# Kernel tuning notes

Measured on AMD Instinct MI355X. Metric: run time of the kernel, lower is better.

Reference implementation:

```python
import jax, jax.numpy as jnp
import numpy as np
import math

B, S, D, L, FF = 16, 2048, 512, 4, 2048
VOCAB, ATTR_VOCAB, MAXPOS = 33, 608, 2048
EPS = 1e-5


def layernorm(x, w, b):
    mu = jnp.mean(x, axis=-1, keepdims=True)
    var = jnp.mean(jnp.square(x - mu), axis=-1, keepdims=True)
    return (x - mu) * jax.lax.rsqrt(var + EPS) * w + b


def setup_inputs() -> dict:
    key = jax.random.key(0)
    ks = jax.random.split(key, 16)
    std = 0.02
    return {
        "input_ids": jax.random.randint(ks[0], (B, S), 0, VOCAB),
        "combined_indices": jax.random.randint(ks[1], (B,), 0, ATTR_VOCAB),
        "attention_mask": jnp.ones((B, S), dtype=jnp.float32),
        "tok_emb": jax.random.normal(ks[2], (VOCAB, D), jnp.float32) * std,
        "pos_emb": jax.random.normal(ks[3], (MAXPOS, D), jnp.float32) * std,
        "attr_emb": jax.random.normal(ks[4], (ATTR_VOCAB, D), jnp.float32) * std,
        "ln_w": jnp.ones((L, D), jnp.float32),
        "ln_b": jnp.zeros((L, D), jnp.float32),
        "w1": jax.random.normal(ks[5], (L, D, FF), jnp.float32) * std,
        "b1": jnp.zeros((L, FF), jnp.float32),
        "w2": jax.random.normal(ks[6], (L, FF, D), jnp.float32) * std,
        "b2": jnp.zeros((L, D), jnp.float32),
        "out_w": jax.random.normal(ks[7], (D, VOCAB), jnp.float32) * std,
        "out_b": jnp.zeros((VOCAB,), jnp.float32),
    }


def reference(input_ids, combined_indices, attention_mask, tok_emb, pos_emb,
              attr_emb, ln_w, ln_b, w1, b1, w2, b2, out_w, out_b):
    scale = 1.0 / math.sqrt(D)
    # embeddings: token + position + per-example attribute (broadcast over seq)
    x = tok_emb[input_ids] + pos_emb[jnp.arange(S)][None, :, :] \
        + attr_emb[combined_indices][:, None, :]
    mask_add = (1.0 - attention_mask)[:, None, :] * -1e9  # [B,1,S]
    for l in range(L):
        h = layernorm(x, ln_w[l], ln_b[l])                 # shared LN params used twice
        scores = jnp.einsum('bsd,btd->bst', h, h) * scale + mask_add
        probs = jax.nn.softmax(scores, axis=-1)            # dropout=0 (eval)
        attn = jnp.einsum('bst,btd->bsd', probs, h) + x    # residual
        n2 = layernorm(attn, ln_w[l], ln_b[l])
        ff = jax.nn.gelu(n2 @ w1[l] + b1[l], approximate=False) @ w2[l] + b2[l]
        x = ff + attn
    return x @ out_w + out_b
```

## Files before the change

kernel.cpp:

```cpp
#include <hip/hip_runtime.h>
#include <hip/hip_bf16.h>
#include <cmath>

#define B_ 16
#define S_ 2048
#define D_ 512
#define L_ 4
#define FF_ 2048
#define V_ 33

typedef unsigned short u16;
typedef __attribute__((ext_vector_type(8))) short bf16x8;
typedef __attribute__((ext_vector_type(4))) float f32x4;

__device__ __forceinline__ u16 f2bf(float f) {
    unsigned x = __float_as_uint(f);
    unsigned r = (x + 0x7fffu + ((x >> 16) & 1u)) >> 16;
    return (u16)r;
}
__device__ __forceinline__ float bf2f(u16 u) { return __uint_as_float(((unsigned)u) << 16); }

__device__ __forceinline__ float wave_sum(float v) {
#pragma unroll
    for (int o = 32; o; o >>= 1) v += __shfl_xor(v, o);
    return v;
}

__device__ __forceinline__ void gload16(const u16* g, u16* l) {
    __builtin_amdgcn_global_load_lds((const __attribute__((address_space(1))) void*)g,
                                     (__attribute__((address_space(3))) void*)l, 16, 0, 0);
}

__device__ __forceinline__ uint4 pack8(const u16* ov) {
    uint4 p;
    p.x = (unsigned)ov[0] | ((unsigned)ov[1] << 16);
    p.y = (unsigned)ov[2] | ((unsigned)ov[3] << 16);
    p.z = (unsigned)ov[4] | ((unsigned)ov[5] << 16);
    p.w = (unsigned)ov[6] | ((unsigned)ov[7] << 16);
    return p;
}

__global__ __launch_bounds__(256) void embed_kernel(
    const int* __restrict__ ids, const int* __restrict__ attr,
    const float* __restrict__ tok, const float* __restrict__ pos,
    const float* __restrict__ attre, float* __restrict__ x)
{
    int idx = blockIdx.x * 256 + threadIdx.x;
    const int total = B_ * S_ * (D_ / 4);
    if (idx >= total) return;
    int d4 = idx & (D_ / 4 - 1);
    int bs = idx >> 7;
    int s  = bs & (S_ - 1);
    int b  = bs >> 11;
    int id = ids[bs];
    int a  = attr[b];
    float4 t  = ((const float4*)tok)[id * (D_ / 4) + d4];
    float4 p  = ((const float4*)pos)[s * (D_ / 4) + d4];
    float4 at = ((const float4*)attre)[a * (D_ / 4) + d4];
    float4 o;
    o.x = t.x + p.x + at.x; o.y = t.y + p.y + at.y;
    o.z = t.z + p.z + at.z; o.w = t.w + p.w + at.w;
    ((float4*)x)[idx] = o;
}

__global__ __launch_bounds__(256) void ln_kernel(
    const float* __restrict__ in, u16* __restrict__ out,
    const float* __restrict__ w, const float* __restrict__ b, int rows)
{
    int gw = (int)((blockIdx.x * 256 + threadIdx.x) >> 6);
    int lane = threadIdx.x & 63;
    if (gw >= rows) return;
    const float4* p = (const float4*)(in + (size_t)gw * D_);
    float4 a0 = p[lane * 2], a1 = p[lane * 2 + 1];
    float xv[8] = {a0.x, a0.y, a0.z, a0.w, a1.x, a1.y, a1.z, a1.w};
    float s = 0.f;
#pragma unroll
    for (int k = 0; k < 8; k++) s += xv[k];
    s = wave_sum(s);
    float mu = s * (1.f / D_);
    float q = 0.f;
#pragma unroll
    for (int k = 0; k < 8; k++) { float d = xv[k] - mu; q += d * d; }
    q = wave_sum(q);
    float rs = rsqrtf(q * (1.f / D_) + 1e-5f);
    const float4* w4 = (const float4*)w;
    const float4* b4 = (const float4*)b;
    float4 w0 = w4[lane * 2], w1v = w4[lane * 2 + 1];
    float4 b0 = b4[lane * 2], b1v = b4[lane * 2 + 1];
    float wv[8] = {w0.x, w0.y, w0.z, w0.w, w1v.x, w1v.y, w1v.z, w1v.w};
    float bv[8] = {b0.x, b0.y, b0.z, b0.w, b1v.x, b1v.y, b1v.z, b1v.w};
    u16 ov[8];
#pragma unroll
    for (int k = 0; k < 8; k++) ov[k] = f2bf((xv[k] - mu) * rs * wv[k] + bv[k]);
    *(uint4*)(out + (size_t)gw * D_ + lane * 8) = pack8(ov);
}

#define LTS 66
__global__ __launch_bounds__(1024) void lnT_kernel(
    const float* __restrict__ in, u16* __restrict__ h, u16* __restrict__ hT,
    const float* __restrict__ w, const float* __restrict__ b)
{
    __shared__ u16 tile[512 * LTS];
    const int tid = threadIdx.x, lane = tid & 63, wv = tid >> 6;
    const int rb = blockIdx.x;
    const int z  = rb >> 5;
    const int s0 = (rb & 31) * 64;

    float wv8[8], bv8[8];
#pragma unroll
    for (int k = 0; k < 8; k++) {
        wv8[k] = w[k * 64 + lane];
        bv8[k] = b[k * 64 + lane];
    }

#pragma unroll
    for (int i = 0; i < 4; i++) {
        const int rl = wv * 4 + i;
        const size_t grow = (size_t)rb * 64 + rl;
        const float* xr = in + grow * D_;
        float xv[8];
#pragma unroll
        for (int k = 0; k < 8; k++) xv[k] = xr[k * 64 + lane];
        float s = 0.f;
#pragma unroll
        for (int k = 0; k < 8; k++) s += xv[k];
        s = wave_sum(s);
        float mu = s * (1.f / D_);
        float q = 0.f;
#pragma unroll
        for (int k = 0; k < 8; k++) { float d = xv[k] - mu; q += d * d; }
        q = wave_sum(q);
        float rs = rsqrtf(q * (1.f / D_) + 1e-5f);
        u16* hr = h + grow * D_;
#pragma unroll
        for (int k = 0; k < 8; k++) {
            u16 v = f2bf((xv[k] - mu) * rs * wv8[k] + bv8[k]);
            hr[k * 64 + lane] = v;
            tile[(k * 64 + lane) * LTS + rl] = v;
        }
    }
    __syncthreads();
    u16* hb = hT + (size_t)z * S_ * D_;
#pragma unroll
    for (int it = 0; it < 4; it++) {
        int idx = it * 1024 + tid;
        int d = idx >> 3, sg = (idx & 7) << 3;
        u16 v[8];
#pragma unroll
        for (int i = 0; i < 8; i++) v[i] = tile[d * LTS + sg + i];
        *(uint4*)(hb + (size_t)d * S_ + s0 + sg) = pack8(v);
    }
}

__device__ __forceinline__ void ld2(const float* p, int idx, u16& a, u16& b) {
    float2 v = ((const float2*)p)[idx];
    a = f2bf(v.x); b = f2bf(v.y);
}
__device__ __forceinline__ void ld2(const u16* p, int idx, u16& a, u16& b) {
    unsigned v = ((const unsigned*)p)[idx];
    a = (u16)(v & 0xffff); b = (u16)(v >> 16);
}

template <typename T>
__global__ void transpose64(const T* __restrict__ in, u16* __restrict__ out,
                            int R, int C, size_t sIn, size_t sOut)
{
    __shared__ u16 tile[64][66];
    const T* ip = in + (size_t)blockIdx.z * sIn;
    u16* op = out + (size_t)blockIdx.z * sOut;
    const int tx = threadIdx.x, ty = threadIdx.y;
#pragma unroll
    for (int i = 0; i < 8; i++) {
        int r = blockIdx.y * 64 + ty + i * 8;
        u16 a, b;
        ld2(ip + (size_t)r * C, blockIdx.x * 32 + tx, a, b);
        tile[tx * 2 + 0][ty + i * 8] = a;
        tile[tx * 2 + 1][ty + i * 8] = b;
    }
    __syncthreads();
#pragma unroll
    for (int i = 0; i < 8; i++) {
        int ocl = ty + i * 8;
        int oc  = blockIdx.x * 64 + ocl;
        unsigned w = (unsigned)tile[ocl][tx * 2] | ((unsigned)tile[ocl][tx * 2 + 1] << 16);
        ((unsigned*)(op + (size_t)oc * R + blockIdx.y * 64))[tx] = w;
    }
}

enum { E_PV = 1, E_GELU = 2, E_FF2 = 3 };

template <int EPI>
__global__ __launch_bounds__(256) void gemm_nt(
    const u16* __restrict__ A, size_t sAz, int lda,
    const u16* __restrict__ B, size_t sBz, int ldb,
    float* Cf, u16* Cb, size_t sCz, int ldc,
    int K, float scale,
    const float* resid, size_t sRz,
    const float* __restrict__ bias,
    const float* __restrict__ aux, int b0)
{
    __shared__ __align__(16) u16 ldsA[128 * 64];
    __shared__ __align__(16) u16 ldsB[128 * 64];
    __shared__ float l2[EPI == E_PV ? 128 : 1][2];

    const int gx = gridDim.x, gy = gridDim.y;
    const int nwg = gx * gy * gridDim.z;
    int lid = blockIdx.x + gx * (blockIdx.y + gy * blockIdx.z);
    {
        const int q = nwg >> 3, r = nwg & 7;
        const int xcd = lid & 7, idx = lid >> 3;
        lid = (xcd < r ? xcd * (q + 1) : r * (q + 1) + (xcd - r) * q) + idx;
    }
    const int bx = lid % gx;
    const int t2 = lid / gx;
    const int by = t2 % gy;
    const int z  = t2 / gy;

    A += (size_t)z * sAz;
    B += (size_t)z * sBz;
    const size_t coff = (size_t)z * sCz;
    const int brow = by * 128, bcol = bx * 128;
    const int tid = threadIdx.x, lane = tid & 63, wid = tid >> 6;
    const int wr = wid >> 1, wc = wid & 1;

    if constexpr (EPI == E_PV) {
        const int nrows = b0;
        const int base = z * S_ + brow;
        const int r = tid >> 1, ih = (tid & 1) << 4;
        float s = 0.f;
#pragma unroll
        for (int i = 0; i < 16; i++)
            s += aux[(size_t)(ih + i) * nrows + base + r];
        l2[r][tid & 1] = s;
    }

    f32x4 acc[4][4];
#pragma unroll
    for (int m = 0; m < 4; m++)
#pragma unroll
        for (int n = 0; n < 4; n++) acc[m][n] = 0.0f;

    const int lg   = lane >> 3;
    const int srow = wid * 8 + lg;
    const int skk  = ((lane & 7) ^ lg) << 3;
    const int l15 = lane & 15, l7 = lane & 7, kh = lane >> 4;

    for (int k0 = 0; k0 < K; k0 += 64) {
        __syncthreads();
#pragma unroll
        for (int r = 0; r < 4; r++) {
            const u16* ga = A + (size_t)(brow + r * 32 + srow) * lda + (k0 + skk);
            const u16* gb = B + (size_t)(bcol + r * 32 + srow) * ldb + (k0 + skk);
            gload16(ga, &ldsA[r * 2048 + wid * 512]);
            gload16(gb, &ldsB[r * 2048 + wid * 512]);
        }
        __syncthreads();
#pragma unroll
        for (int kk = 0; kk < 64; kk += 32) {
            const int kc = (kk >> 3) + kh;
            const int kswz = ((kc ^ l7) << 3);
            bf16x8 af[4], bfv[4];
#pragma unroll
            for (int m = 0; m < 4; m++)
                af[m] = *(const bf16x8*)&ldsA[(wr * 64 + m * 16 + l15) * 64 + kswz];
#pragma unroll
            for (int n = 0; n < 4; n++)
                bfv[n] = *(const bf16x8*)&ldsB[(wc * 64 + n * 16 + l15) * 64 + kswz];
#pragma unroll
            for (int m = 0; m < 4; m++)
#pragma unroll
                for (int n = 0; n < 4; n++)
                    acc[m][n] = __builtin_amdgcn_mfma_f32_16x16x32_bf16(af[m], bfv[n], acc[m][n], 0, 0, 0);
        }
    }

#pragma unroll
    for (int m = 0; m < 4; m++)
#pragma unroll
        for (int n = 0; n < 4; n++) {
            int rowb = brow + wr * 64 + m * 16 + ((lane >> 4) << 2);
            int col  = bcol + wc * 64 + n * 16 + l15;
#pragma unroll
            for (int j = 0; j < 4; j++) {
                int row = rowb + j;
                float v = acc[m][n][j];
                size_t off = coff + (size_t)row * ldc + col;
                if constexpr (EPI == E_PV) {
                    int rl = row - brow;
                    float lv = l2[rl][0] + l2[rl][1];
                    Cf[off] = v / lv + resid[(size_t)z * sRz + (size_t)row * ldc + col];
                } else if constexpr (EPI == E_GELU) {
                    float t = v + bias[col];
                    Cb[off] = f2bf(0.5f * t * (1.f + erff(t * 0.70710678118f)));
                } else {
                    Cf[off] = v + bias[col] + resid[(size_t)row * ldc + col];
                }
            }
        }
}

__global__ __launch_bounds__(256) void gemm_sc(
    const u16* __restrict__ h, u16* __restrict__ P,
    const float* __restrict__ mask, int b0, float scale,
    float* __restrict__ psum, int nbatch)
{
    __shared__ __align__(16) u16 ldsbuf[2][128 * 64];
    u16* ldsA = ldsbuf[0];
    u16* ldsB = ldsbuf[1];
    u16* mt   = &ldsbuf[0][0];

    const int nwg = 136 * nbatch;
    int lid = blockIdx.x + 136 * blockIdx.z;
    {
        const int q = nwg >> 3, r = nwg & 7;
        const int xcd = lid & 7, idx = lid >> 3;
        lid = (xcd < r ? xcd * (q + 1) : r * (q + 1) + (xcd - r) * q) + idx;
    }
    int t = lid % 136;
    const int z = lid / 136;
    int by = 0;
#pragma unroll 1
    while (t >= 16 - by) { t -= 16 - by; by++; }
    const int bx = by + t;

    const u16* A = h + (size_t)z * S_ * D_;
    const size_t coff = (size_t)z * S_ * S_;
    const int brow = by * 128, bcol = bx * 128;
    const int tid = threadIdx.x, lane = tid & 63, wid = tid >> 6;
    const int wr = wid >> 1, wc = wid & 1;

    f32x4 acc[4][4];
#pragma unroll
    for (int m = 0; m < 4; m++)
#pragma unroll
        for (int n = 0; n < 4; n++) acc[m][n] = 0.0f;

    const int lg   = lane >> 3;
    const int srow = wid * 8 + lg;
    const int skk  = ((lane & 7) ^ lg) << 3;
    const int l15 = lane & 15, l7 = lane & 7, kh = lane >> 4;

    for (int k0 = 0; k0 < D_; k0 += 64) {
        __syncthreads();
#pragma unroll
        for (int r = 0; r < 4; r++) {
            const u16* ga = A + (size_t)(brow + r * 32 + srow) * D_ + (k0 + skk);
            const u16* gb = A + (size_t)(bcol + r * 32 + srow) * D_ + (k0 + skk);
            gload16(ga, &ldsA[r * 2048 + wid * 512]);
            gload16(gb, &ldsB[r * 2048 + wid * 512]);
        }
        __syncthreads();
#pragma unroll
        for (int kk = 0; kk < 64; kk += 32) {
            const int kc = (kk >> 3) + kh;
            const int kswz = ((kc ^ l7) << 3);
            bf16x8 af[4], bfv[4];
#pragma unroll
            for (int m = 0; m < 4; m++)
                af[m] = *(const bf16x8*)&ldsA[(wr * 64 + m * 16 + l15) * 64 + kswz];
#pragma unroll
            for (int n = 0; n < 4; n++)
                bfv[n] = *(const bf16x8*)&ldsB[(wc * 64 + n * 16 + l15) * 64 + kswz];
#pragma unroll
            for (int m = 0; m < 4; m++)
#pragma unroll
                for (int n = 0; n < 4; n++)
                    acc[m][n] = __builtin_amdgcn_mfma_f32_16x16x32_bf16(af[m], bfv[n], acc[m][n], 0, 0, 0);
        }
    }

    const float* mrow = mask + (size_t)(b0 + z) * S_;
    const int nrows = nbatch * S_;

    float rsum[4][4];
#pragma unroll
    for (int m = 0; m < 4; m++)
#pragma unroll
        for (int j = 0; j < 4; j++) rsum[m][j] = 0.f;

#pragma unroll
    for (int m = 0; m < 4; m++)
#pragma unroll
        for (int n = 0; n < 4; n++) {
            int rowb = brow + wr * 64 + m * 16 + (kh << 2);
            int col  = bcol + wc * 64 + n * 16 + l15;
            float madd_c = (1.f - mrow[col]) * -1e9f;
#pragma unroll
            for (int j = 0; j < 4; j++) {
                int row = rowb + j;
                float ev = __expf(acc[m][n][j] * scale + madd_c);
                P[coff + (size_t)row * S_ + col] = f2bf(ev);
                rsum[m][j] += ev;
            }
        }
#pragma unroll
    for (int m = 0; m < 4; m++) {
        int rowl = brow + wr * 64 + m * 16 + (kh << 2);
#pragma unroll
        for (int j = 0; j < 4; j++) {
            float s = rsum[m][j];
            s += __shfl_xor(s, 1);
            s += __shfl_xor(s, 2);
            s += __shfl_xor(s, 4);
            s += __shfl_xor(s, 8);
            if (l15 == 0)
                psum[(size_t)(bx * 2 + wc) * nrows + (size_t)z * S_ + rowl + j] = s;
        }
    }

    if (bx != by) {
#pragma unroll 1
        for (int rnd = 0; rnd < 2; rnd++) {
            __syncthreads();
            if (wc == rnd) {
#pragma unroll
                for (int n = 0; n < 4; n++) {
                    float csum = 0.f;
                    const int mrow_l = n * 16 + l15;
#pragma unroll
                    for (int m = 0; m < 4; m++) {
                        const int lr = wr * 64 + m * 16 + (kh << 2);
                        u16 e2[4];
#pragma unroll
                        for (int j = 0; j < 4; j++) {
                            float madd_r = (1.f - mrow[brow + lr + j]) * -1e9f;
                            float em = __expf(acc[m][n][j] * scale + madd_r);
                            csum += em;
                            e2[j] = f2bf(em);
                        }
                        unsigned* m32 = (unsigned*)&mt[mrow_l * 136 + lr];
                        m32[0] = (unsigned)e2[0] | ((unsigned)e2[1] << 16);
                        m32[1] = (unsigned)e2[2] | ((unsigned)e2[3] << 16);
                    }
                    csum += __shfl_xor(csum, 16);
                    csum += __shfl_xor(csum, 32);
                    if (lane < 16)
                        psum[(size_t)(by * 2 + wr) * nrows + (size_t)z * S_ +
                             bcol + rnd * 64 + n * 16 + lane] = csum;
                }
            }
            __syncthreads();
#pragma unroll 1
            for (int i = tid; i < 64 * 16; i += 256) {
                int rr = i >> 4, c16 = (i & 15) << 3;
                u16 v[8];
#pragma unroll
                for (int q = 0; q < 8; q++) v[q] = mt[rr * 136 + c16 + q];
                *(uint4*)(P + coff + (size_t)(bcol + rnd * 64 + rr) * S_ + brow + c16) = pack8(v);
            }
        }
    }
}

__global__ __launch_bounds__(256) void wtb_kernel(
    const float* __restrict__ W, u16* __restrict__ WTb)
{
    int i = blockIdx.x * 256 + threadIdx.x;
    if (i >= 64 * 512) return;
    int n = i >> 9, k = i & 511;
    WTb[i] = f2bf(n < V_ ? W[k * V_ + n] : 0.f);
}

__global__ __launch_bounds__(256) void outproj_mfma(
    const float* __restrict__ x, const u16* __restrict__ WTb,
    const float* __restrict__ bias, float* __restrict__ out)
{
    __shared__ __align__(16) u16 ldsA[128 * 64];
    __shared__ __align__(16) u16 ldsB[64 * 64];
    __shared__ float obuf[128][34];
    const int brow = blockIdx.x * 128;
    const int tid = threadIdx.x, lane = tid & 63, wid = tid >> 6;
    const int wr = wid >> 1, wc = wid & 1;
    const int l15 = lane & 15, l7 = lane & 7, kh = lane >> 4;
    const int lg = lane >> 3, srow = wid * 8 + lg;
    const int skk = ((lane & 7) ^ lg) << 3;
    const int ar = tid >> 1, ah = (tid & 1) * 32;

    f32x4 acc[4][2];
#pragma unroll
    for (int m = 0; m < 4; m++)
#pragma unroll
        for (int n = 0; n < 2; n++) acc[m][n] = 0.0f;

    for (int k0 = 0; k0 < 512; k0 += 64) {
        __syncthreads();
#pragma unroll
        for (int r = 0; r < 2; r++)
            gload16(WTb + (size_t)(r * 32 + srow) * 512 + (k0 + skk),
                    &ldsB[r * 2048 + wid * 512]);
        const float4* xs = (const float4*)(x + (size_t)(brow + ar) * 512 + k0 + ah);
#pragma unroll
        for (int j = 0; j < 4; j++) {
            float4 a = xs[j * 2], b = xs[j * 2 + 1];
            u16 t[8] = {f2bf(a.x), f2bf(a.y), f2bf(a.z), f2bf(a.w),
                        f2bf(b.x), f2bf(b.y), f2bf(b.z), f2bf(b.w)};
            int kc = (ah >> 3) + j;
            *(uint4*)&ldsA[ar * 64 + ((kc ^ (ar & 7)) << 3)] = pack8(t);
        }
        __syncthreads();
#pragma unroll
        for (int kk = 0; kk < 64; kk += 32) {
            const int kc = (kk >> 3) + kh;
            const int kswz = ((kc ^ l7) << 3);
            bf16x8 af[4], bfv[2];
#pragma unroll
            for (int m = 0; m < 4; m++)
                af[m] = *(const bf16x8*)&ldsA[(wr * 64 + m * 16 + l15) * 64 + kswz];
#pragma unroll
            for (int n = 0; n < 2; n++)
                bfv[n] = *(const bf16x8*)&ldsB[(wc * 32 + n * 16 + l15) * 64 + kswz];
#pragma unroll
            for (int m = 0; m < 4; m++)
#pragma unroll
                for (int n = 0; n < 2; n++)
                    acc[m][n] = __builtin_amdgcn_mfma_f32_16x16x32_bf16(af[m], bfv[n], acc[m][n], 0, 0, 0);
        }
    }

#pragma unroll
    for (int m = 0; m < 4; m++)
#pragma unroll
        for (int n = 0; n < 2; n++) {
            int rowl = wr * 64 + m * 16 + ((lane >> 4) << 2);
            int col  = wc * 32 + n * 16 + l15;
            if (col < V_) {
#pragma unroll
                for (int j = 0; j < 4; j++)
                    obuf[rowl + j][col] = acc[m][n][j] + bias[col];
            }
        }
    __syncthreads();
    float* ob = out + (size_t)brow * V_;
#pragma unroll 1
    for (int i = tid; i < 128 * V_; i += 256)
        ob[i] = obuf[i / V_][i % V_];
}

extern "C" void kernel_launch(void* const* d_in, const int* in_sizes, int n_in,
                              void* d_out, int out_size, void* d_ws, size_t ws_size,
                              hipStream_t stream)
{
    const int*   input_ids = (const int*)d_in[0];
    const int*   comb      = (const int*)d_in[1];
    const float* amask     = (const float*)d_in[2];
    const float* tok       = (const float*)d_in[3];
    const float* pos       = (const float*)d_in[4];
    const float* attre     = (const float*)d_in[5];
    const float* ln_w      = (const float*)d_in[6];
    const float* ln_b      = (const float*)d_in[7];
    const float* w1        = (const float*)d_in[8];
    const float* b1        = (const float*)d_in[9];
    const float* w2        = (const float*)d_in[10];
    const float* b2        = (const float*)d_in[11];
    const float* out_w     = (const float*)d_in[12];
    const float* out_b     = (const float*)d_in[13];
    float* out = (float*)d_out;
    (void)in_sizes; (void)n_in; (void)out_size;

    int NB_A, RC;
    if      (ws_size >= 335000000ULL) { NB_A = 16; RC = 32768; }
    else if (ws_size >= 215000000ULL) { NB_A = 8;  RC = 16384; }
    else if (ws_size >= 152000000ULL) { NB_A = 4;  RC = 8192;  }
    else                              { NB_A = 2;  RC = 4096;  }
    const int HR = NB_A * S_;

    unsigned char* ws = (unsigned char*)d_ws;
    size_t off = 0;
    auto carve = [&](size_t bytes) {
        void* p = ws + off;
        off += (bytes + 255) & ~(size_t)255;
        return p;
    };
    float* x    = (float*)carve((size_t)B_ * S_ * D_ * 4);
    u16* w1t    = (u16*)carve((size_t)L_ * D_ * FF_ * 2);
    u16* w2t    = (u16*)carve((size_t)L_ * D_ * FF_ * 2);
    u16* h      = (u16*)carve((size_t)HR * D_ * 2);
    u16* hT     = (u16*)carve((size_t)NB_A * S_ * D_ * 2);
    float* psum = (float*)carve((size_t)NB_A * S_ * 32 * 4);
    u16* WTb    = (u16*)carve((size_t)64 * 512 * 2);
    size_t scP_bytes  = (size_t)NB_A * S_ * S_ * 2;
    size_t tbuf_bytes = (size_t)RC * FF_ * 2;
    void* un = carve(scP_bytes > tbuf_bytes ? scP_bytes : tbuf_bytes);
    u16* scP  = (u16*)un;
    u16* tbuf = (u16*)un;

    const float scl = 1.0f / sqrtf((float)D_);
    const int nG = B_ / NB_A;
    const int nC = (B_ * S_) / RC;

    embed_kernel<<<(B_ * S_ * (D_ / 4)) / 256, 256, 0, stream>>>(input_ids, comb, tok, pos, attre, x);
    transpose64<float><<<dim3(FF_ / 64, D_ / 64, L_), dim3(32, 8), 0, stream>>>(
        w1, w1t, D_, FF_, (size_t)D_ * FF_, (size_t)FF_ * D_);
    transpose64<float><<<dim3(D_ / 64, FF_ / 64, L_), dim3(32, 8), 0, stream>>>(
        w2, w2t, FF_, D_, (size_t)FF_ * D_, (size_t)D_ * FF_);
    wtb_kernel<<<128, 256, 0, stream>>>(out_w, WTb);

    for (int l = 0; l < L_; l++) {
        const float* lw = ln_w + l * D_;
        const float* lb = ln_b + l * D_;

        for (int g = 0; g < nG; g++) {
            float* xg = x + (size_t)g * NB_A * S_ * D_;
            lnT_kernel<<<(NB_A * S_) / 64, 1024, 0, stream>>>(xg, h, hT, lw, lb);
            gemm_sc<<<dim3(136, 1, NB_A), 256, 0, stream>>>(
                h, scP, amask, g * NB_A, scl, psum, NB_A);
            gemm_nt<E_PV><<<dim3(D_ / 128, S_ / 128, NB_A), 256, 0, stream>>>(
                scP, (size_t)S_ * S_, S_,
                hT, (size_t)S_ * D_, S_,
                xg, nullptr, (size_t)S_ * D_, D_,
                S_, 1.f, xg, (size_t)S_ * D_, nullptr, psum, NB_A * S_);
        }

        for (int c = 0; c < nC; c++) {
            size_t roff = (size_t)c * RC;
            ln_kernel<<<RC / 4, 256, 0, stream>>>(x + roff * D_, h, lw, lb, RC);
            gemm_nt<E_GELU><<<dim3(FF_ / 128, RC / 128, 1), 256, 0, stream>>>(
                h, 0, D_,
                w1t + (size_t)l * FF_ * D_, 0, D_,
                nullptr, tbuf, 0, FF_,
                D_, 1.f, nullptr, 0, b1 + l * FF_, nullptr, 0);
            gemm_nt<E_FF2><<<dim3(D_ / 128, RC / 128, 1), 256, 0, stream>>>(
                tbuf, 0, FF_,
                w2t + (size_t)l * D_ * FF_, 0, FF_,
                x + roff * D_, nullptr, 0, D_,
                FF_, 1.f, x + roff * D_, 0, b2 + l * D_, nullptr, 0);
        }
    }

    outproj_mfma<<<(B_ * S_) / 128, 256, 0, stream>>>(x, WTb, out_b, out);
}
```

Baseline: 2.005 ms.

## Store residual stream in bf16 instead of fp32

Switches the residual activation buffer x from fp32 to bf16 across the embed, layernorm, PV epilogue, FF2 epilogue and output projection. The output projection now loads x directly into LDS with async global loads instead of converting on the fly. Halving the residual buffer also lowers the workspace thresholds, so larger attention batch and FFN chunk sizes can be chosen. This cuts memory traffic on x, but rounding the residual to bf16 at every layer adds accumulated error relative to the fp32 reference.

```diff
diff --git a/kernel.cpp b/kernel.cpp
--- a/kernel.cpp
+++ b/kernel.cpp
@@ -43,36 +43,45 @@
 __global__ __launch_bounds__(256) void embed_kernel(
     const int* __restrict__ ids, const int* __restrict__ attr,
     const float* __restrict__ tok, const float* __restrict__ pos,
-    const float* __restrict__ attre, float* __restrict__ x)
+    const float* __restrict__ attre, u16* __restrict__ x)
 {
     int idx = blockIdx.x * 256 + threadIdx.x;
-    const int total = B_ * S_ * (D_ / 4);
+    const int total = B_ * S_ * (D_ / 8);
     if (idx >= total) return;
-    int d4 = idx & (D_ / 4 - 1);
-    int bs = idx >> 7;
+    int d8 = idx & (D_ / 8 - 1);
+    int bs = idx >> 6;
     int s  = bs & (S_ - 1);
     int b  = bs >> 11;
     int id = ids[bs];
     int a  = attr[b];
-    float4 t  = ((const float4*)tok)[id * (D_ / 4) + d4];
-    float4 p  = ((const float4*)pos)[s * (D_ / 4) + d4];
-    float4 at = ((const float4*)attre)[a * (D_ / 4) + d4];
-    float4 o;
-    o.x = t.x + p.x + at.x; o.y = t.y + p.y + at.y;
-    o.z = t.z + p.z + at.z; o.w = t.w + p.w + at.w;
-    ((float4*)x)[idx] = o;
+    const float4* t4 = (const float4*)(tok   + (size_t)id * D_) + d8 * 2;
+    const float4* p4 = (const float4*)(pos   + (size_t)s  * D_) + d8 * 2;
+    const float4* a4 = (const float4*)(attre + (size_t)a  * D_) + d8 * 2;
+    u16 ov[8];
+#pragma unroll
+    for (int h = 0; h < 2; h++) {
+        float4 t = t4[h], p = p4[h], at = a4[h];
+        ov[h * 4 + 0] = f2bf(t.x + p.x + at.x);
+        ov[h * 4 + 1] = f2bf(t.y + p.y + at.y);
+        ov[h * 4 + 2] = f2bf(t.z + p.z + at.z);
+        ov[h * 4 + 3] = f2bf(t.w + p.w + at.w);
+    }
+    *(uint4*)(x + (size_t)idx * 8) = pack8(ov);
 }
 
 __global__ __launch_bounds__(256) void ln_kernel(
-    const float* __restrict__ in, u16* __restrict__ out,
+    const u16* __restrict__ in, u16* __restrict__ out,
     const float* __restrict__ w, const float* __restrict__ b, int rows)
 {
     int gw = (int)((blockIdx.x * 256 + threadIdx.x) >> 6);
     int lane = threadIdx.x & 63;
     if (gw >= rows) return;
-    const float4* p = (const float4*)(in + (size_t)gw * D_);
-    float4 a0 = p[lane * 2], a1 = p[lane * 2 + 1];
-    float xv[8] = {a0.x, a0.y, a0.z, a0.w, a1.x, a1.y, a1.z, a1.w};
+    uint4 pk = *(const uint4*)(in + (size_t)gw * D_ + lane * 8);
+    float xv[8];
+    xv[0] = bf2f((u16)(pk.x & 0xffff)); xv[1] = bf2f((u16)(pk.x >> 16));
+    xv[2] = bf2f((u16)(pk.y & 0xffff)); xv[3] = bf2f((u16)(pk.y >> 16));
+    xv[4] = bf2f((u16)(pk.z & 0xffff)); xv[5] = bf2f((u16)(pk.z >> 16));
+    xv[6] = bf2f((u16)(pk.w & 0xffff)); xv[7] = bf2f((u16)(pk.w >> 16));
     float s = 0.f;
 #pragma unroll
     for (int k = 0; k < 8; k++) s += xv[k];
@@ -97,7 +106,7 @@
 
 #define LTS 66
 __global__ __launch_bounds__(1024) void lnT_kernel(
-    const float* __restrict__ in, u16* __restrict__ h, u16* __restrict__ hT,
+    const u16* __restrict__ in, u16* __restrict__ h, u16* __restrict__ hT,
     const float* __restrict__ w, const float* __restrict__ b)
 {
     __shared__ u16 tile[512 * LTS];
@@ -117,10 +126,10 @@
     for (int i = 0; i < 4; i++) {
         const int rl = wv * 4 + i;
         const size_t grow = (size_t)rb * 64 + rl;
-        const float* xr = in + grow * D_;
+        const u16* xr = in + grow * D_;
         float xv[8];
 #pragma unroll
-        for (int k = 0; k < 8; k++) xv[k] = xr[k * 64 + lane];
+        for (int k = 0; k < 8; k++) xv[k] = bf2f(xr[k * 64 + lane]);
         float s = 0.f;
 #pragma unroll
         for (int k = 0; k < 8; k++) s += xv[k];
@@ -156,17 +165,12 @@
     float2 v = ((const float2*)p)[idx];
     a = f2bf(v.x); b = f2bf(v.y);
 }
-__device__ __forceinline__ void ld2(const u16* p, int idx, u16& a, u16& b) {
-    unsigned v = ((const unsigned*)p)[idx];
-    a = (u16)(v & 0xffff); b = (u16)(v >> 16);
-}
-
-template <typename T>
-__global__ void transpose64(const T* __restrict__ in, u16* __restrict__ out,
+
+__global__ void transpose64(const float* __restrict__ in, u16* __restrict__ out,
                             int R, int C, size_t sIn, size_t sOut)
 {
     __shared__ u16 tile[64][66];
-    const T* ip = in + (size_t)blockIdx.z * sIn;
+    const float* ip = in + (size_t)blockIdx.z * sIn;
     u16* op = out + (size_t)blockIdx.z * sOut;
     const int tx = threadIdx.x, ty = threadIdx.y;
 #pragma unroll
@@ -193,9 +197,9 @@
 __global__ __launch_bounds__(256) void gemm_nt(
     const u16* __restrict__ A, size_t sAz, int lda,
     const u16* __restrict__ B, size_t sBz, int ldb,
-    float* Cf, u16* Cb, size_t sCz, int ldc,
-    int K, float scale,
-    const float* resid, size_t sRz,
+    u16* Cb, size_t sCz, int ldc,
+    int K,
+    const u16* resid, size_t sRz,
     const float* __restrict__ bias,
     const float* __restrict__ aux, int b0)
 {
@@ -288,12 +292,14 @@
                 if constexpr (EPI == E_PV) {
                     int rl = row - brow;
                     float lv = l2[rl][0] + l2[rl][1];
-                    Cf[off] = v / lv + resid[(size_t)z * sRz + (size_t)row * ldc + col];
+                    Cb[off] = f2bf(v / lv +
+                                   bf2f(resid[(size_t)z * sRz + (size_t)row * ldc + col]));
                 } else if constexpr (EPI == E_GELU) {
                     float t = v + bias[col];
                     Cb[off] = f2bf(0.5f * t * (1.f + erff(t * 0.70710678118f)));
                 } else {
-                    Cf[off] = v + bias[col] + resid[(size_t)row * ldc + col];
+                    Cb[off] = f2bf(v + bias[col] +
+                                   bf2f(resid[(size_t)row * ldc + col]));
                 }
             }
         }
@@ -462,7 +468,7 @@
 }
 
 __global__ __launch_bounds__(256) void outproj_mfma(
-    const float* __restrict__ x, const u16* __restrict__ WTb,
+    const u16* __restrict__ x, const u16* __restrict__ WTb,
     const float* __restrict__ bias, float* __restrict__ out)
 {
     __shared__ __align__(16) u16 ldsA[128 * 64];
@@ -474,7 +480,6 @@
     const int l15 = lane & 15, l7 = lane & 7, kh = lane >> 4;
     const int lg = lane >> 3, srow = wid * 8 + lg;
     const int skk = ((lane & 7) ^ lg) << 3;
-    const int ar = tid >> 1, ah = (tid & 1) * 32;
 
     f32x4 acc[4][2];
 #pragma unroll
@@ -488,15 +493,10 @@
         for (int r = 0; r < 2; r++)
             gload16(WTb + (size_t)(r * 32 + srow) * 512 + (k0 + skk),
                     &ldsB[r * 2048 + wid * 512]);
-        const float4* xs = (const float4*)(x + (size_t)(brow + ar) * 512 + k0 + ah);
-#pragma unroll
-        for (int j = 0; j < 4; j++) {
-            float4 a = xs[j * 2], b = xs[j * 2 + 1];
-            u16 t[8] = {f2bf(a.x), f2bf(a.y), f2bf(a.z), f2bf(a.w),
-                        f2bf(b.x), f2bf(b.y), f2bf(b.z), f2bf(b.w)};
-            int kc = (ah >> 3) + j;
-            *(uint4*)&ldsA[ar * 64 + ((kc ^ (ar & 7)) << 3)] = pack8(t);
-        }
+#pragma unroll
+        for (int r = 0; r < 4; r++)
+            gload16(x + (size_t)(brow + r * 32 + srow) * 512 + (k0 + skk),
+                    &ldsA[r * 2048 + wid * 512]);
         __syncthreads();
 #pragma unroll
         for (int kk = 0; kk < 64; kk += 32) {
@@ -558,9 +558,9 @@
     (void)in_sizes; (void)n_in; (void)out_size;
 
     int NB_A, RC;
-    if      (ws_size >= 335000000ULL) { NB_A = 16; RC = 32768; }
-    else if (ws_size >= 215000000ULL) { NB_A = 8;  RC = 16384; }
-    else if (ws_size >= 152000000ULL) { NB_A = 4;  RC = 8192;  }
+    if      (ws_size >= 300000000ULL) { NB_A = 16; RC = 32768; }
+    else if (ws_size >= 180000000ULL) { NB_A = 8;  RC = 16384; }
+    else if (ws_size >= 120000000ULL) { NB_A = 4;  RC = 8192;  }
     else                              { NB_A = 2;  RC = 4096;  }
     const int HR = NB_A * S_;
 
@@ -571,7 +571,7 @@
         off += (bytes + 255) & ~(size_t)255;
         return p;
     };
-    float* x    = (float*)carve((size_t)B_ * S_ * D_ * 4);
+    u16* x      = (u16*)carve((size_t)B_ * S_ * D_ * 2);
     u16* w1t    = (u16*)carve((size_t)L_ * D_ * FF_ * 2);
     u16* w2t    = (u16*)carve((size_t)L_ * D_ * FF_ * 2);
     u16* h      = (u16*)carve((size_t)HR * D_ * 2);
@@ -588,10 +588,10 @@
     const int nG = B_ / NB_A;
     const int nC = (B_ * S_) / RC;
 
-    embed_kernel<<<(B_ * S_ * (D_ / 4)) / 256, 256, 0, stream>>>(input_ids, comb, tok, pos, attre, x);
-    transpose64<float><<<dim3(FF_ / 64, D_ / 64, L_), dim3(32, 8), 0, stream>>>(
+    embed_kernel<<<(B_ * S_ * (D_ / 8)) / 256, 256, 0, stream>>>(input_ids, comb, tok, pos, attre, x);
+    transpose64<<<dim3(FF_ / 64, D_ / 64, L_), dim3(32, 8), 0, stream>>>(
         w1, w1t, D_, FF_, (size_t)D_ * FF_, (size_t)FF_ * D_);
-    transpose64<float><<<dim3(D_ / 64, FF_ / 64, L_), dim3(32, 8), 0, stream>>>(
+    transpose64<<<dim3(D_ / 64, FF_ / 64, L_), dim3(32, 8), 0, stream>>>(
         w2, w2t, FF_, D_, (size_t)FF_ * D_, (size_t)D_ * FF_);
     wtb_kernel<<<128, 256, 0, stream>>>(out_w, WTb);
 
@@ -600,15 +600,15 @@
         const float* lb = ln_b + l * D_;
 
         for (int g = 0; g < nG; g++) {
-            float* xg = x + (size_t)g * NB_A * S_ * D_;
+            u16* xg = x + (size_t)g * NB_A * S_ * D_;
             lnT_kernel<<<(NB_A * S_) / 64, 1024, 0, stream>>>(xg, h, hT, lw, lb);
             gemm_sc<<<dim3(136, 1, NB_A), 256, 0, stream>>>(
                 h, scP, amask, g * NB_A, scl, psum, NB_A);
             gemm_nt<E_PV><<<dim3(D_ / 128, S_ / 128, NB_A), 256, 0, stream>>>(
                 scP, (size_t)S_ * S_, S_,
                 hT, (size_t)S_ * D_, S_,
-                xg, nullptr, (size_t)S_ * D_, D_,
-                S_, 1.f, xg, (size_t)S_ * D_, nullptr, psum, NB_A * S_);
+                xg, (size_t)S_ * D_, D_,
+                S_, xg, (size_t)S_ * D_, nullptr, psum, NB_A * S_);
         }
 
         for (int c = 0; c < nC; c++) {
@@ -617,13 +617,13 @@
             gemm_nt<E_GELU><<<dim3(FF_ / 128, RC / 128, 1), 256, 0, stream>>>(
                 h, 0, D_,
                 w1t + (size_t)l * FF_ * D_, 0, D_,
-                nullptr, tbuf, 0, FF_,
-                D_, 1.f, nullptr, 0, b1 + l * FF_, nullptr, 0);
+                tbuf, 0, FF_,
+                D_, nullptr, 0, b1 + l * FF_, nullptr, 0);
             gemm_nt<E_FF2><<<dim3(D_ / 128, RC / 128, 1), 256, 0, stream>>>(
                 tbuf, 0, FF_,
                 w2t + (size_t)l * D_ * FF_, 0, FF_,
-                x + roff * D_, nullptr, 0, D_,
-                FF_, 1.f, x + roff * D_, 0, b2 + l * D_, nullptr, 0);
+                x + roff * D_, 0, D_,
+                FF_, x + roff * D_, 0, b2 + l * D_, nullptr, 0);
         }
     }
 
```

Result: faster. 1.905 ms, median of 2 (-5.0%).
